# Kernel tuning notes

Measured on AMD Instinct MI355X. Metric: run time of the kernel, lower is better.

The kernel has to match this reference:

```python
import jax, jax.numpy as jnp
import numpy as np

B, H, S, D = 4, 16, 2048, 64
TEMPERATURE = 8.0  # sqrt(D)
NEG = -1000000000.0

def setup_inputs() -> dict:
    key = jax.random.key(0)
    kq, kk, kv, km = jax.random.split(key, 4)
    q = jax.random.normal(kq, (B, H, S, D), dtype=jnp.float32)
    k = jax.random.normal(kk, (B, H, S, D), dtype=jnp.float32)
    v = jax.random.normal(kv, (B, H, S, D), dtype=jnp.float32)
    mask = jax.random.randint(km, (B, 1, S, S), 0, 2, dtype=jnp.int32)
    return {"q": q, "k": k, "v": v, "mask": mask}

def reference(q, k, v, mask):
    # scores: [B,H,S,S]
    scores = jnp.einsum('bhqd,bhkd->bhqk', q / TEMPERATURE, k)
    scores = jnp.where(mask == 1, NEG, scores)
    attn = jax.nn.softmax(scores, axis=-1)  # dropout p=0.0 -> identity
    out = jnp.einsum('bhqk,bhkd->bhqd', attn, v)
    return out
```

## Files before the change

kernel.cpp:

```cpp
#include <hip/hip_runtime.h>

#define NB 4
#define NH 16
#define SS 2048
#define DD 64
#define QT 256
#define KT 64
#define NT (SS / KT)
#define KSP 72
#define QSCALE 0.18033688011112042f

#define WS_BITS_BYTES ((size_t)NB * SS * (SS / 8))
#define WS_KB_OFF  ((size_t)2  << 20)
#define WS_VB_OFF  ((size_t)18 << 20)
#define WS_FULL    ((size_t)34 << 20)

typedef __bf16 bf16x8 __attribute__((ext_vector_type(8)));
typedef __bf16 bf16x2 __attribute__((ext_vector_type(2)));
typedef float  floatx16 __attribute__((ext_vector_type(16)));
typedef unsigned long long u64t;

static_assert(sizeof(bf16x8) == 16, "bf16x8 must be 16B");

__device__ __forceinline__ int pack2(float a, float b) {
    bf16x2 v; v[0] = (__bf16)a; v[1] = (__bf16)b;
    return __builtin_bit_cast(int, v);
}

__device__ __forceinline__ int vperm_col(int k) {
    return 16 * (k >> 4) + 8 * ((k >> 2) & 1) + (k & 3) + 4 * ((k >> 3) & 1);
}
__device__ __forceinline__ int vperm_inv(int c) {
    return 16 * ((c >> 4) & 3) + 8 * ((c >> 2) & 1) + 4 * ((c >> 3) & 1) + (c & 3);
}

__global__ __launch_bounds__(256)
void pack_mask_kernel(const int* __restrict__ M, u64t* __restrict__ bits)
{
    const int w    = (blockIdx.x * 256 + threadIdx.x) >> 6;
    const int lane = threadIdx.x & 63;
    #pragma unroll 4
    for (int i = 0; i < 32; ++i) {
        const int gw   = i * 8192 + w;
        const size_t row = (size_t)(gw >> 5);
        const int word = gw & 31;
        const int mval = M[row * SS + (size_t)word * 64 + lane];
        const u64t b = __ballot(mval == 1);
        if (lane == 0) bits[gw] = b;
    }
}

__global__ __launch_bounds__(256)
void pre_kernel(const float* __restrict__ K, const float* __restrict__ V,
                const int* __restrict__ M, u64t* __restrict__ bits,
                __bf16* __restrict__ KB, __bf16* __restrict__ VB)
{
    __shared__ float vt[64][68];
    const int t = threadIdx.x;

    if (blockIdx.x < 2048) {
        const int bh = blockIdx.x >> 5;
        const int tt = blockIdx.x & 31;
        const size_t tb = (size_t)bh * SS * DD + (size_t)tt * (KT * DD);

        {
            const float* src = K + tb + t * 16;
            __bf16* dst = KB + tb + t * 16;
            float4 f0 = ((const float4*)src)[0];
            float4 f1 = ((const float4*)src)[1];
            float4 f2 = ((const float4*)src)[2];
            float4 f3 = ((const float4*)src)[3];
            bf16x8 o0, o1;
            o0[0]=(__bf16)f0.x; o0[1]=(__bf16)f0.y; o0[2]=(__bf16)f0.z; o0[3]=(__bf16)f0.w;
            o0[4]=(__bf16)f1.x; o0[5]=(__bf16)f1.y; o0[6]=(__bf16)f1.z; o0[7]=(__bf16)f1.w;
            o1[0]=(__bf16)f2.x; o1[1]=(__bf16)f2.y; o1[2]=(__bf16)f2.z; o1[3]=(__bf16)f2.w;
            o1[4]=(__bf16)f3.x; o1[5]=(__bf16)f3.y; o1[6]=(__bf16)f3.z; o1[7]=(__bf16)f3.w;
            ((bf16x8*)dst)[0] = o0;
            ((bf16x8*)dst)[1] = o1;
        }

        {
            const int key = t >> 2, ds = (t & 3) * 16;
            const float* src = V + tb + (size_t)key * DD + ds;
            #pragma unroll
            for (int i = 0; i < 4; ++i)
                *(float4*)&vt[key][ds + 4 * i] = ((const float4*)src)[i];
        }
        __syncthreads();
        {
            const int dim = t >> 2, cb = (t & 3) * 16;
            bf16x8 o0, o1;
            #pragma unroll
            for (int c = 0; c < 16; ++c) {
                const float vvv = vt[vperm_inv(cb + c)][dim];
                if (c < 8) o0[c] = (__bf16)vvv; else o1[c - 8] = (__bf16)vvv;
            }
            __bf16* dst = VB + tb + (size_t)dim * 64 + cb;
            ((bf16x8*)dst)[0] = o0;
            ((bf16x8*)dst)[1] = o1;
        }
    } else {
        const int w    = ((blockIdx.x - 2048) * 256 + t) >> 6;
        const int lane = t & 63;
        #pragma unroll 4
        for (int i = 0; i < 32; ++i) {
            const int gw   = i * 8192 + w;
            const size_t row = (size_t)(gw >> 5);
            const int word = gw & 31;
            const int mval = M[row * SS + (size_t)word * 64 + lane];
            const u64t b = __ballot(mval == 1);
            if (lane == 0) bits[gw] = b;
        }
    }
}

template<int MODE>
__global__ __launch_bounds__(512, 4)
void attn_kernel(const float* __restrict__ Q, const float* __restrict__ K,
                 const float* __restrict__ V, const int* __restrict__ M,
                 const unsigned* __restrict__ MB,
                 const __bf16* __restrict__ KB, const __bf16* __restrict__ VB,
                 float* __restrict__ O)
{
    __shared__ __bf16 ks [2][KT][KSP];
    __shared__ __bf16 vsT[2][DD][KSP];

    const int t    = threadIdx.x;
    const int wave = t >> 6;
    const int lane = t & 63;
    const int l31  = lane & 31;
    const int h8   = lane >> 5;

    const int bh    = blockIdx.x & 63;
    const int qtile = blockIdx.x >> 6;
    const int b     = bh >> 4;
    const int q0    = qtile * QT + wave * 32;

    const size_t base = (size_t)bh * SS * DD;

    bf16x8 aq[4];
    {
        const float* qp = Q + base + (size_t)(q0 + l31) * DD + 8 * h8;
        #pragma unroll
        for (int s = 0; s < 4; ++s) {
            float4 f0 = *(const float4*)(qp + 16 * s);
            float4 f1 = *(const float4*)(qp + 16 * s + 4);
            bf16x8 a;
            a[0] = (__bf16)(f0.x * QSCALE); a[1] = (__bf16)(f0.y * QSCALE);
            a[2] = (__bf16)(f0.z * QSCALE); a[3] = (__bf16)(f0.w * QSCALE);
            a[4] = (__bf16)(f1.x * QSCALE); a[5] = (__bf16)(f1.y * QSCALE);
            a[6] = (__bf16)(f1.z * QSCALE); a[7] = (__bf16)(f1.w * QSCALE);
            aq[s] = a;
        }
    }

    const int srow = t >> 3;
    const int sc8  = (t & 7) * 8;
    const __bf16* kbp = KB + base + (size_t)srow * DD + sc8;
    const __bf16* vbp = VB + base + (size_t)srow * DD + sc8;
    bf16x8 kreg, vreg;

    const int skey = t >> 3;
    const int sdc  = (t & 7) * 8;
    const int vk   = 2 * (t & 31);
    const int vdc  = (t >> 5) * 4;
    const int vcol = vperm_col(vk);
    const float* kp0 = K + base + (size_t)skey * DD + sdc;
    const float* vp0 = V + base + (size_t)vk * DD + vdc;
    float4 ka0, ka1, va0, va1;

    if constexpr (MODE == 2) {
        kreg = *(const bf16x8*)kbp;
        vreg = *(const bf16x8*)vbp;
    } else {
        ka0 = ((const float4*)kp0)[0];
        ka1 = ((const float4*)kp0)[1];
        va0 = *(const float4*)(vp0);
        va1 = *(const float4*)(vp0 + DD);
    }

    const u64t* mbrow = (const u64t*)MB + ((size_t)b * SS + q0 + l31) * (SS / 64);
    const int*  mrow  = M + (size_t)b * SS * SS + (size_t)(q0 + l31) * SS + 4 * h8;

    floatx16 o0, o1;
    #pragma unroll
    for (int i = 0; i < 16; ++i) { o0[i] = 0.f; o1[i] = 0.f; }
    float ls = 0.f;

    for (int tt = 0; tt < NT; ++tt) {
        const int cur = tt & 1;

        if constexpr (MODE == 2) {
            *(bf16x8*)&ks [cur][srow][sc8] = kreg;
            *(bf16x8*)&vsT[cur][srow][sc8] = vreg;
        } else {
            bf16x8 kw;
            kw[0]=(__bf16)ka0.x; kw[1]=(__bf16)ka0.y; kw[2]=(__bf16)ka0.z; kw[3]=(__bf16)ka0.w;
            kw[4]=(__bf16)ka1.x; kw[5]=(__bf16)ka1.y; kw[6]=(__bf16)ka1.z; kw[7]=(__bf16)ka1.w;
            *(bf16x8*)&ks[cur][skey][sdc] = kw;
            #pragma unroll
            for (int i = 0; i < 4; ++i) {
                bf16x2 pr;
                pr[0] = (__bf16)(&va0.x)[i]; pr[1] = (__bf16)(&va1.x)[i];
                *(bf16x2*)&vsT[cur][vdc + i][vcol] = pr;
            }
        }
        __syncthreads();

        u64t mall = 0;
        int4 mi[8];
        if constexpr (MODE >= 1) {
            mall = mbrow[tt];
        } else {
            #pragma unroll
            for (int g = 0; g < 8; ++g)
                mi[g] = *(const int4*)(mrow + tt * KT + 8 * g);
        }

        if constexpr (MODE == 2) {
            const size_t jn = (size_t)((tt + 1) & (NT - 1)) * (KT * DD);
            kreg = *(const bf16x8*)(kbp + jn);
            vreg = *(const bf16x8*)(vbp + jn);
        } else {
            const int jn = ((tt + 1) * KT) & (SS - 1);
            const float* kn = kp0 + (size_t)jn * DD;
            ka0 = ((const float4*)kn)[0];
            ka1 = ((const float4*)kn)[1];
            const float* vn = vp0 + (size_t)jn * DD;
            va0 = *(const float4*)(vn);
            va1 = *(const float4*)(vn + DD);
        }

        #pragma unroll
        for (int half = 0; half < 2; ++half) {
            floatx16 c;
            #pragma unroll
            for (int i = 0; i < 16; ++i) c[i] = 0.f;
            __builtin_amdgcn_s_setprio(1);
            #pragma unroll
            for (int s = 0; s < 4; ++s) {
                bf16x8 a = *(const bf16x8*)&ks[cur][32 * half + l31][16 * s + 8 * h8];
                c = __builtin_amdgcn_mfma_f32_32x32x16_bf16(a, aq[s], c, 0, 0, 0);
            }
            __builtin_amdgcn_s_setprio(0);

            const unsigned mw = (MODE >= 1) ? (unsigned)(mall >> (32 * half)) : 0u;
            const unsigned u  = mw >> (4 * h8);
            int pk[8];
            float psum = 0.f;
            #pragma unroll
            for (int g = 0; g < 8; ++g) {
                const int ia = 2 * g, ib = 2 * g + 1;
                float pa = __builtin_amdgcn_exp2f(c[ia]);
                float pb = __builtin_amdgcn_exp2f(c[ib]);
                bool ma, mb_;
                if constexpr (MODE >= 1) {
                    ma  = (u >> ((ia & 3) + 8 * (ia >> 2))) & 1;
                    mb_ = (u >> ((ib & 3) + 8 * (ib >> 2))) & 1;
                } else {
                    const int g2 = 4 * half + (ia >> 2);
                    ma  = ((&mi[g2].x)[ia & 3] == 1);
                    mb_ = ((&mi[g2].x)[ib & 3] == 1);
                }
                pa = ma  ? 0.f : pa;
                pb = mb_ ? 0.f : pb;
                psum += pa + pb;
                pk[g] = pack2(pa, pb);
            }
            ls += psum;

            __builtin_amdgcn_s_setprio(1);
            #pragma unroll
            for (int s2 = 0; s2 < 2; ++s2) {
                int4 fw; fw.x = pk[4*s2]; fw.y = pk[4*s2+1]; fw.z = pk[4*s2+2]; fw.w = pk[4*s2+3];
                bf16x8 bp = __builtin_bit_cast(bf16x8, fw);
                bf16x8 av0 = *(const bf16x8*)&vsT[cur][l31]     [32 * half + 16 * s2 + 8 * h8];
                bf16x8 av1 = *(const bf16x8*)&vsT[cur][32 + l31][32 * half + 16 * s2 + 8 * h8];
                o0 = __builtin_amdgcn_mfma_f32_32x32x16_bf16(av0, bp, o0, 0, 0, 0);
                o1 = __builtin_amdgcn_mfma_f32_32x32x16_bf16(av1, bp, o1, 0, 0, 0);
            }
            __builtin_amdgcn_s_setprio(0);
        }
    }

    ls += __shfl_xor(ls, 32);
    float inv = 1.0f / ls;
    float* op = O + base + (size_t)(q0 + l31) * DD;
    #pragma unroll
    for (int s = 0; s < 4; ++s) {
        float4 st0, st1;
        st0.x = o0[4*s+0] * inv; st0.y = o0[4*s+1] * inv;
        st0.z = o0[4*s+2] * inv; st0.w = o0[4*s+3] * inv;
        st1.x = o1[4*s+0] * inv; st1.y = o1[4*s+1] * inv;
        st1.z = o1[4*s+2] * inv; st1.w = o1[4*s+3] * inv;
        *(float4*)(op + 8 * s + 4 * h8)      = st0;
        *(float4*)(op + 32 + 8 * s + 4 * h8) = st1;
    }
}

extern "C" void kernel_launch(void* const* d_in, const int* in_sizes, int n_in,
                              void* d_out, int out_size, void* d_ws, size_t ws_size,
                              hipStream_t stream) {
    (void)in_sizes; (void)n_in; (void)out_size;
    const float* q = (const float*)d_in[0];
    const float* k = (const float*)d_in[1];
    const float* v = (const float*)d_in[2];
    const int*   m = (const int*)d_in[3];
    float* out = (float*)d_out;
    dim3 grid(NB * NH * (SS / QT));

    if (ws_size >= WS_FULL) {
        u64t*   bits = (u64t*)d_ws;
        __bf16* kb16 = (__bf16*)((char*)d_ws + WS_KB_OFF);
        __bf16* vb16 = (__bf16*)((char*)d_ws + WS_VB_OFF);
        pre_kernel<<<dim3(4096), 256, 0, stream>>>(k, v, m, bits, kb16, vb16);
        attn_kernel<2><<<grid, 512, 0, stream>>>(q, k, v, m, (const unsigned*)bits,
                                                 kb16, vb16, out);
    } else if (ws_size >= WS_BITS_BYTES) {
        u64t* bits = (u64t*)d_ws;
        pack_mask_kernel<<<dim3(2048), 256, 0, stream>>>(m, bits);
        attn_kernel<1><<<grid, 512, 0, stream>>>(q, k, v, m, (const unsigned*)bits,
                                                 nullptr, nullptr, out);
    } else {
        attn_kernel<0><<<grid, 512, 0, stream>>>(q, k, v, m, nullptr,
                                                 nullptr, nullptr, out);
    }
}
```

Measured before the change: 273.6 us.

## Fold mask into MFMA accumulator init and compute row sums via ones-MFMA

The MFMA accumulator for the scores is now initialised to a large negative bias (-1024) wherever the mask bit is set, so exp2 yields zero directly and the per-element select is gone. The softmax denominator is accumulated by an extra MFMA against a vector of ones instead of scalar adds plus a cross-lane shuffle. The next tile's mask word is prefetched one iteration ahead, and the mask-packing grid is doubled with half the iterations per block. The cost is one extra MFMA per PV step, and the row sum is now built from bf16-rounded probabilities.

```diff
diff --git a/kernel.cpp b/kernel.cpp
--- a/kernel.cpp
+++ b/kernel.cpp
@@ -27,9 +27,6 @@
     return __builtin_bit_cast(int, v);
 }
 
-__device__ __forceinline__ int vperm_col(int k) {
-    return 16 * (k >> 4) + 8 * ((k >> 2) & 1) + (k & 3) + 4 * ((k >> 3) & 1);
-}
 __device__ __forceinline__ int vperm_inv(int c) {
     return 16 * ((c >> 4) & 3) + 8 * ((c >> 2) & 1) + 4 * ((c >> 3) & 1) + (c & 3);
 }
@@ -40,8 +37,8 @@
     const int w    = (blockIdx.x * 256 + threadIdx.x) >> 6;
     const int lane = threadIdx.x & 63;
     #pragma unroll 4
-    for (int i = 0; i < 32; ++i) {
-        const int gw   = i * 8192 + w;
+    for (int i = 0; i < 16; ++i) {
+        const int gw   = i * 16384 + w;
         const size_t row = (size_t)(gw >> 5);
         const int word = gw & 31;
         const int mval = M[row * SS + (size_t)word * 64 + lane];
@@ -103,8 +100,8 @@
         const int w    = ((blockIdx.x - 2048) * 256 + t) >> 6;
         const int lane = t & 63;
         #pragma unroll 4
-        for (int i = 0; i < 32; ++i) {
-            const int gw   = i * 8192 + w;
+        for (int i = 0; i < 16; ++i) {
+            const int gw   = i * 16384 + w;
             const size_t row = (size_t)(gw >> 5);
             const int word = gw & 31;
             const int mval = M[row * SS + (size_t)word * 64 + lane];
@@ -154,6 +151,10 @@
         }
     }
 
+    bf16x8 ones8;
+    #pragma unroll
+    for (int i = 0; i < 8; ++i) ones8[i] = (__bf16)1.0f;
+
     const int srow = t >> 3;
     const int sc8  = (t & 7) * 8;
     const __bf16* kbp = KB + base + (size_t)srow * DD + sc8;
@@ -164,7 +165,7 @@
     const int sdc  = (t & 7) * 8;
     const int vk   = 2 * (t & 31);
     const int vdc  = (t >> 5) * 4;
-    const int vcol = vperm_col(vk);
+    const int vcol = 16 * (vk >> 4) + 8 * ((vk >> 2) & 1) + (vk & 3) + 4 * ((vk >> 3) & 1);
     const float* kp0 = K + base + (size_t)skey * DD + sdc;
     const float* vp0 = V + base + (size_t)vk * DD + vdc;
     float4 ka0, ka1, va0, va1;
@@ -181,11 +182,12 @@
 
     const u64t* mbrow = (const u64t*)MB + ((size_t)b * SS + q0 + l31) * (SS / 64);
     const int*  mrow  = M + (size_t)b * SS * SS + (size_t)(q0 + l31) * SS + 4 * h8;
-
-    floatx16 o0, o1;
+    u64t mall = 0, mnext = 0;
+    if constexpr (MODE >= 1) mall = mbrow[0];
+
+    floatx16 o0, o1, oL;
     #pragma unroll
-    for (int i = 0; i < 16; ++i) { o0[i] = 0.f; o1[i] = 0.f; }
-    float ls = 0.f;
+    for (int i = 0; i < 16; ++i) { o0[i] = 0.f; o1[i] = 0.f; oL[i] = 0.f; }
 
     for (int tt = 0; tt < NT; ++tt) {
         const int cur = tt & 1;
@@ -207,11 +209,8 @@
         }
         __syncthreads();
 
-        u64t mall = 0;
         int4 mi[8];
-        if constexpr (MODE >= 1) {
-            mall = mbrow[tt];
-        } else {
+        if constexpr (MODE == 0) {
             #pragma unroll
             for (int g = 0; g < 8; ++g)
                 mi[g] = *(const int4*)(mrow + tt * KT + 8 * g);
@@ -230,12 +229,27 @@
             va0 = *(const float4*)(vn);
             va1 = *(const float4*)(vn + DD);
         }
+        if constexpr (MODE >= 1) mnext = mbrow[(tt + 1) & (NT - 1)];
 
         #pragma unroll
         for (int half = 0; half < 2; ++half) {
             floatx16 c;
-            #pragma unroll
-            for (int i = 0; i < 16; ++i) c[i] = 0.f;
+            if constexpr (MODE >= 1) {
+                const unsigned u = (unsigned)(mall >> (32 * half)) >> (4 * h8);
+                #pragma unroll
+                for (int i = 0; i < 16; ++i) {
+                    const int pos = (i & 3) + 8 * (i >> 2);
+                    const int sm = ((int)(u << (31 - pos))) >> 31;
+                    c[i] = __builtin_bit_cast(float, sm & (int)0xC4800000u);
+                }
+            } else {
+                #pragma unroll
+                for (int i = 0; i < 16; ++i) {
+                    const int g2 = 4 * half + (i >> 2);
+                    c[i] = ((&mi[g2].x)[i & 3] == 1) ? -1024.0f : 0.0f;
+                }
+            }
+
             __builtin_amdgcn_s_setprio(1);
             #pragma unroll
             for (int s = 0; s < 4; ++s) {
@@ -244,30 +258,13 @@
             }
             __builtin_amdgcn_s_setprio(0);
 
-            const unsigned mw = (MODE >= 1) ? (unsigned)(mall >> (32 * half)) : 0u;
-            const unsigned u  = mw >> (4 * h8);
             int pk[8];
-            float psum = 0.f;
             #pragma unroll
             for (int g = 0; g < 8; ++g) {
-                const int ia = 2 * g, ib = 2 * g + 1;
-                float pa = __builtin_amdgcn_exp2f(c[ia]);
-                float pb = __builtin_amdgcn_exp2f(c[ib]);
-                bool ma, mb_;
-                if constexpr (MODE >= 1) {
-                    ma  = (u >> ((ia & 3) + 8 * (ia >> 2))) & 1;
-                    mb_ = (u >> ((ib & 3) + 8 * (ib >> 2))) & 1;
-                } else {
-                    const int g2 = 4 * half + (ia >> 2);
-                    ma  = ((&mi[g2].x)[ia & 3] == 1);
-                    mb_ = ((&mi[g2].x)[ib & 3] == 1);
-                }
-                pa = ma  ? 0.f : pa;
-                pb = mb_ ? 0.f : pb;
-                psum += pa + pb;
+                float pa = __builtin_amdgcn_exp2f(c[2 * g]);
+                float pb = __builtin_amdgcn_exp2f(c[2 * g + 1]);
                 pk[g] = pack2(pa, pb);
             }
-            ls += psum;
 
             __builtin_amdgcn_s_setprio(1);
             #pragma unroll
@@ -278,13 +275,15 @@
                 bf16x8 av1 = *(const bf16x8*)&vsT[cur][32 + l31][32 * half + 16 * s2 + 8 * h8];
                 o0 = __builtin_amdgcn_mfma_f32_32x32x16_bf16(av0, bp, o0, 0, 0, 0);
                 o1 = __builtin_amdgcn_mfma_f32_32x32x16_bf16(av1, bp, o1, 0, 0, 0);
+                oL = __builtin_amdgcn_mfma_f32_32x32x16_bf16(ones8, bp, oL, 0, 0, 0);
             }
             __builtin_amdgcn_s_setprio(0);
         }
-    }
-
-    ls += __shfl_xor(ls, 32);
-    float inv = 1.0f / ls;
+
+        if constexpr (MODE >= 1) mall = mnext;
+    }
+
+    float inv = 1.0f / oL[0];
     float* op = O + base + (size_t)(q0 + l31) * DD;
     #pragma unroll
     for (int s = 0; s < 4; ++s) {
@@ -313,12 +312,12 @@
         u64t*   bits = (u64t*)d_ws;
         __bf16* kb16 = (__bf16*)((char*)d_ws + WS_KB_OFF);
         __bf16* vb16 = (__bf16*)((char*)d_ws + WS_VB_OFF);
-        pre_kernel<<<dim3(4096), 256, 0, stream>>>(k, v, m, bits, kb16, vb16);
+        pre_kernel<<<dim3(6144), 256, 0, stream>>>(k, v, m, bits, kb16, vb16);
         attn_kernel<2><<<grid, 512, 0, stream>>>(q, k, v, m, (const unsigned*)bits,
                                                  kb16, vb16, out);
     } else if (ws_size >= WS_BITS_BYTES) {
         u64t* bits = (u64t*)d_ws;
-        pack_mask_kernel<<<dim3(2048), 256, 0, stream>>>(m, bits);
+        pack_mask_kernel<<<dim3(4096), 256, 0, stream>>>(m, bits);
         attn_kernel<1><<<grid, 512, 0, stream>>>(q, k, v, m, (const unsigned*)bits,
                                                  nullptr, nullptr, out);
     } else {
```

Result: no change. 272.1 us (-0.6%).
